# Optimization experiments

Measured on AMD Instinct MI355X. Metric: run time of the kernel, lower is better.

The kernel has to match this reference:

```python
import jax, jax.numpy as jnp
from jax import lax
import numpy as np
import math

N = 8
IN_CH = 3
EPS = 1e-6


def _dct_basis(n=N):
    # basis[u, i] = c(u) * cos(pi * u * (i + 0.5) / n)
    u = np.arange(n)
    i = np.arange(n)
    b = np.cos(np.pi * np.outer(u, i + 0.5) / n)
    c = np.full(n, math.sqrt(2.0 / n))
    c[0] = math.sqrt(1.0 / n)
    return b * c[:, None]


def _dct_conv_weight(n=N, in_ch=IN_CH):
    # weight[k = u*n + v, i, j] = basis[u,i] * basis[v,j]; grouped conv OIHW with I=1
    b = _dct_basis(n)
    w = np.einsum('ui,vj->uvij', b, b).reshape(n * n, 1, n, n).astype(np.float32)
    return np.concatenate([w] * in_ch, axis=0)  # [in_ch*n*n, 1, n, n]


def setup_inputs() -> dict:
    key = jax.random.key(0)
    k1, k2, k3 = jax.random.split(key, 3)
    B, C, H, W = 32, 3, 512, 512
    x = jax.random.uniform(k1, (B, C, H, W), dtype=jnp.float32)  # RGB in [0,1)
    # per-(sample, channel) stats; keep divisor d = max - min + eps > 1 so the
    # B-times repeated in-place normalization of the original stays finite
    max_ = 1.5 + jax.random.uniform(k2, (B, C * N * N, 1, 1), dtype=jnp.float32)
    min_ = 0.1 * jax.random.uniform(k3, (B, C * N * N, 1, 1), dtype=jnp.float32)
    ycbcr_w = jnp.asarray(
        [[0.299, 0.587, 0.114],
         [-0.169, -0.331, 0.5],
         [0.5, -0.419, -0.081]], dtype=jnp.float32)  # [out_c, in_c]
    dct_w = jnp.asarray(_dct_conv_weight())  # [192, 1, 8, 8]
    return {"x": x, "max_": max_, "min_": min_, "ycbcr_w": ycbcr_w, "dct_w": dct_w}


def reference(x, max_, min_, ycbcr_w, dct_w):
    # 1x1 RGB -> YCbCr conv == channel matmul
    ycbcr = jnp.einsum('oc,bchw->bohw', ycbcr_w, x)
    # grouped 8x8 stride-8 block-DCT conv: [B, 192, H/8, W/8]
    dct = lax.conv_general_dilated(
        ycbcr, dct_w, window_strides=(N, N), padding='VALID',
        feature_group_count=IN_CH,
        dimension_numbers=('NCHW', 'OIHW', 'NCHW'))
    # Original applies t = (t - min) / (max - min + eps) in-place B times per
    # sample (outer loop index i is unused but repeats the whole inner loop).
    d = max_ - min_ + EPS
    B = x.shape[0]
    out = lax.fori_loop(0, B, lambda i, t: (t - min_) / d, dct)
    return out
```

## Files before the change

### kernel.cpp

```cpp
#include <hip/hip_runtime.h>


#define HW 512
#define CHST (HW * HW)
#define NPAIR 6144
#define EPS 1e-6f

static constexpr float BASIS[8][8] = {
  { 0.35355339059327373f, 0.35355339059327373f, 0.35355339059327373f, 0.35355339059327373f,
    0.35355339059327373f, 0.35355339059327373f, 0.35355339059327373f, 0.35355339059327373f },
  { 0.49039264020161522f, 0.41573480615127262f, 0.27778511650980114f, 0.09754516100806412f,
   -0.09754516100806412f,-0.27778511650980114f,-0.41573480615127262f,-0.49039264020161522f },
  { 0.46193976625564337f, 0.19134171618254492f,-0.19134171618254492f,-0.46193976625564337f,
   -0.46193976625564337f,-0.19134171618254492f, 0.19134171618254492f, 0.46193976625564337f },
  { 0.41573480615127262f,-0.09754516100806412f,-0.49039264020161522f,-0.27778511650980114f,
    0.27778511650980114f, 0.49039264020161522f, 0.09754516100806412f,-0.41573480615127262f },
  { 0.35355339059327373f,-0.35355339059327373f,-0.35355339059327373f, 0.35355339059327373f,
    0.35355339059327373f,-0.35355339059327373f,-0.35355339059327373f, 0.35355339059327373f },
  { 0.27778511650980114f,-0.49039264020161522f, 0.09754516100806412f, 0.41573480615127262f,
   -0.41573480615127262f,-0.09754516100806412f, 0.49039264020161522f,-0.27778511650980114f },
  { 0.19134171618254492f,-0.46193976625564337f, 0.46193976625564337f,-0.19134171618254492f,
   -0.19134171618254492f, 0.46193976625564337f,-0.46193976625564337f, 0.19134171618254492f },
  { 0.09754516100806412f,-0.27778511650980114f, 0.41573480615127262f,-0.49039264020161522f,
    0.49039264020161522f,-0.41573480615127262f, 0.27778511650980114f,-0.09754516100806412f }
};

__global__ void precomp_norm(const float* __restrict__ max_,
                             const float* __restrict__ min_,
                             float* __restrict__ so) {
    int i = blockIdx.x * 256 + threadIdx.x;
    if (i >= NPAIR) return;
    float mn = min_[i], mx = max_[i];
    float d = mx - mn + EPS;
    float a = 1.0f / d;
    float a2 = a * a, a4 = a2 * a2, a8 = a4 * a4, a16 = a8 * a8, a32 = a16 * a16;
    float geo = a * (1.0f - a32) / (1.0f - a);
    so[2 * i]     = a32;
    so[2 * i + 1] = -mn * geo;
}

template <bool USE_WS>
__global__ __launch_bounds__(192, 4)
void dct_kernel(const float* __restrict__ x,
                const float* __restrict__ ycbcr_w,
                const float* __restrict__ so,
                const float* __restrict__ max_,
                const float* __restrict__ min_,
                float* __restrict__ out) {
    const int b  = blockIdx.x >> 6;
    const int by = blockIdx.x & 63;
    const int t  = threadIdx.x;
    const int c  = t >> 6;
    const int bx = t & 63;

    const float wr = ycbcr_w[3 * c];
    const float wg = ycbcr_w[3 * c + 1];
    const float wb = ycbcr_w[3 * c + 2];

    const float* base = x + (size_t)(b * 3) * CHST + (size_t)(by * 8) * HW + bx * 8;

    float tmp[8][8];
#pragma unroll
    for (int u = 0; u < 8; ++u)
#pragma unroll
        for (int j = 0; j < 8; ++j) tmp[u][j] = 0.0f;

#pragma unroll
    for (int i = 0; i < 8; ++i) {
        const float* rp = base + i * HW;
        float4 r0 = *(const float4*)(rp);
        float4 r1 = *(const float4*)(rp + 4);
        float4 g0 = *(const float4*)(rp + CHST);
        float4 g1 = *(const float4*)(rp + CHST + 4);
        float4 b0 = *(const float4*)(rp + 2 * CHST);
        float4 b1 = *(const float4*)(rp + 2 * CHST + 4);

        float y[8];
        y[0] = fmaf(wr, r0.x, fmaf(wg, g0.x, wb * b0.x));
        y[1] = fmaf(wr, r0.y, fmaf(wg, g0.y, wb * b0.y));
        y[2] = fmaf(wr, r0.z, fmaf(wg, g0.z, wb * b0.z));
        y[3] = fmaf(wr, r0.w, fmaf(wg, g0.w, wb * b0.w));
        y[4] = fmaf(wr, r1.x, fmaf(wg, g1.x, wb * b1.x));
        y[5] = fmaf(wr, r1.y, fmaf(wg, g1.y, wb * b1.y));
        y[6] = fmaf(wr, r1.z, fmaf(wg, g1.z, wb * b1.z));
        y[7] = fmaf(wr, r1.w, fmaf(wg, g1.w, wb * b1.w));

#pragma unroll
        for (int u = 0; u < 8; ++u) {
            const float bu = BASIS[u][i];
#pragma unroll
            for (int j = 0; j < 8; ++j)
                tmp[u][j] = fmaf(bu, y[j], tmp[u][j]);
        }
    }

    const int obase = b * 192 + c * 64;
    float* op = out + ((size_t)obase * 64 + by) * 64 + bx;
    const float2* sop = (const float2*)so + obase;

#pragma unroll
    for (int u = 0; u < 8; ++u) {
#pragma unroll
        for (int v = 0; v < 8; ++v) {
            float acc = tmp[u][0] * BASIS[v][0];
#pragma unroll
            for (int j = 1; j < 8; ++j)
                acc = fmaf(tmp[u][j], BASIS[v][j], acc);
            const int k = u * 8 + v;
            float s, o;
            if (USE_WS) {
                float2 p = sop[k];
                s = p.x;
                o = p.y;
            } else {
                float mn = min_[obase + k], mx = max_[obase + k];
                float d  = mx - mn + EPS;
                float a  = 1.0f / d;
                float a2 = a * a, a4 = a2 * a2, a8 = a4 * a4, a16 = a8 * a8, a32 = a16 * a16;
                s = a32;
                o = -mn * (a * (1.0f - a32) / (1.0f - a));
            }
            op[(size_t)k * 4096] = fmaf(s, acc, o);
        }
    }
}

extern "C" void kernel_launch(void* const* d_in, const int* in_sizes, int n_in,
                              void* d_out, int out_size, void* d_ws, size_t ws_size,
                              hipStream_t stream) {
    const float* x    = (const float*)d_in[0];
    const float* max_ = (const float*)d_in[1];
    const float* min_ = (const float*)d_in[2];
    const float* yw   = (const float*)d_in[3];
    float* out = (float*)d_out;
    float* so  = (float*)d_ws;

    const bool use_ws = (ws_size >= (size_t)NPAIR * 2 * sizeof(float));
    if (use_ws) {
        precomp_norm<<<(NPAIR + 255) / 256, 256, 0, stream>>>(max_, min_, so);
        dct_kernel<true><<<32 * 64, 192, 0, stream>>>(x, yw, so, max_, min_, out);
    } else {
        dct_kernel<false><<<32 * 64, 192, 0, stream>>>(x, yw, nullptr, max_, min_, out);
    }
}
```

Measured before the change: 202.1 us.

## Split DCT rows across two wavefronts per channel and use nontemporal stores

Each wavefront now computes only half of the u-rows (4 of 8) for one channel. The column transform is applied first and the row accumulation runs only over that half, which halves per-thread accumulator registers so the kernel can target higher occupancy (256 threads, 5 blocks per SM bound). In exchange the input tile is loaded twice and the column DCT is recomputed redundantly by both halves. Output stores become nontemporal so the streamed results do not pollute cache.

```diff
diff --git a/kernel.cpp b/kernel.cpp
--- a/kernel.cpp
+++ b/kernel.cpp
@@ -40,18 +40,21 @@
 }
 
 template <bool USE_WS>
-__global__ __launch_bounds__(192, 4)
+__global__ __launch_bounds__(256, 5)
 void dct_kernel(const float* __restrict__ x,
                 const float* __restrict__ ycbcr_w,
                 const float* __restrict__ so,
                 const float* __restrict__ max_,
                 const float* __restrict__ min_,
                 float* __restrict__ out) {
-    const int b  = blockIdx.x >> 6;
-    const int by = blockIdx.x & 63;
-    const int t  = threadIdx.x;
-    const int c  = t >> 6;
-    const int bx = t & 63;
+    const int wt   = blockIdx.x * 4 + (threadIdx.x >> 6);
+    const int bx   = threadIdx.x & 63;
+    const int band = wt / 6;
+    const int rem  = wt - band * 6;
+    const int c    = rem >> 1;
+    const int uh   = (rem & 1) * 4;
+    const int by   = band & 63;
+    const int b    = band >> 6;
 
     const float wr = ycbcr_w[3 * c];
     const float wg = ycbcr_w[3 * c + 1];
@@ -59,11 +62,11 @@
 
     const float* base = x + (size_t)(b * 3) * CHST + (size_t)(by * 8) * HW + bx * 8;
 
-    float tmp[8][8];
+    float acc[4][8];
 #pragma unroll
-    for (int u = 0; u < 8; ++u)
+    for (int u0 = 0; u0 < 4; ++u0)
 #pragma unroll
-        for (int j = 0; j < 8; ++j) tmp[u][j] = 0.0f;
+        for (int v = 0; v < 8; ++v) acc[u0][v] = 0.0f;
 
 #pragma unroll
     for (int i = 0; i < 8; ++i) {
@@ -85,12 +88,22 @@
         y[6] = fmaf(wr, r1.z, fmaf(wg, g1.z, wb * b1.z));
         y[7] = fmaf(wr, r1.w, fmaf(wg, g1.w, wb * b1.w));
 
+        float z[8];
 #pragma unroll
-        for (int u = 0; u < 8; ++u) {
-            const float bu = BASIS[u][i];
+        for (int v = 0; v < 8; ++v) {
+            float zz = y[0] * BASIS[v][0];
 #pragma unroll
-            for (int j = 0; j < 8; ++j)
-                tmp[u][j] = fmaf(bu, y[j], tmp[u][j]);
+            for (int j = 1; j < 8; ++j)
+                zz = fmaf(y[j], BASIS[v][j], zz);
+            z[v] = zz;
+        }
+
+#pragma unroll
+        for (int u0 = 0; u0 < 4; ++u0) {
+            const float bu = BASIS[uh + u0][i];
+#pragma unroll
+            for (int v = 0; v < 8; ++v)
+                acc[u0][v] = fmaf(bu, z[v], acc[u0][v]);
         }
     }
 
@@ -99,14 +112,10 @@
     const float2* sop = (const float2*)so + obase;
 
 #pragma unroll
-    for (int u = 0; u < 8; ++u) {
+    for (int u0 = 0; u0 < 4; ++u0) {
 #pragma unroll
         for (int v = 0; v < 8; ++v) {
-            float acc = tmp[u][0] * BASIS[v][0];
-#pragma unroll
-            for (int j = 1; j < 8; ++j)
-                acc = fmaf(tmp[u][j], BASIS[v][j], acc);
-            const int k = u * 8 + v;
+            const int k = (uh + u0) * 8 + v;
             float s, o;
             if (USE_WS) {
                 float2 p = sop[k];
@@ -120,7 +129,8 @@
                 s = a32;
                 o = -mn * (a * (1.0f - a32) / (1.0f - a));
             }
-            op[(size_t)k * 4096] = fmaf(s, acc, o);
+            __builtin_nontemporal_store(fmaf(s, acc[u0][v], o),
+                                        op + (size_t)k * 4096);
         }
     }
 }
@@ -138,8 +148,8 @@
     const bool use_ws = (ws_size >= (size_t)NPAIR * 2 * sizeof(float));
     if (use_ws) {
         precomp_norm<<<(NPAIR + 255) / 256, 256, 0, stream>>>(max_, min_, so);
-        dct_kernel<true><<<32 * 64, 192, 0, stream>>>(x, yw, so, max_, min_, out);
+        dct_kernel<true><<<3072, 256, 0, stream>>>(x, yw, so, max_, min_, out);
     } else {
-        dct_kernel<false><<<32 * 64, 192, 0, stream>>>(x, yw, nullptr, max_, min_, out);
+        dct_kernel<false><<<3072, 256, 0, stream>>>(x, yw, nullptr, max_, min_, out);
     }
 }
```

Result: slower. 225.1 us (+11.4%).
